# Optimization experiments

Measured on AMD Instinct MI355X. Metric: run time of the kernel, lower is better.

## Reference

```python
import jax, jax.numpy as jnp
import numpy as np

N_HEADS = 12
ROPE_THETA = 10000.0


def _rope(x):
    # x: [B, L, N, D]; interleaved (lucidrains rotary_embedding_torch style) rotation over full D
    B, L, N, D = x.shape
    inv_freq = 1.0 / (ROPE_THETA ** (jnp.arange(0, D, 2, dtype=jnp.float32) / D))  # [D/2]
    freqs = jnp.arange(L, dtype=jnp.float32)[:, None] * inv_freq                    # [L, D/2]
    cos = jnp.repeat(jnp.cos(freqs), 2, axis=-1)[None, :, None, :].astype(x.dtype)  # [1,L,1,D]
    sin = jnp.repeat(jnp.sin(freqs), 2, axis=-1)[None, :, None, :].astype(x.dtype)
    x1 = x[..., 0::2]
    x2 = x[..., 1::2]
    x_rot = jnp.stack([-x2, x1], axis=-1).reshape(x.shape)  # rotate_half, interleaved pairs
    return x * cos + x_rot * sin


def setup_inputs() -> dict:
    key = jax.random.key(0)
    ks = jax.random.split(key, 7)
    B, L, dm = 8, 1024, 768
    x = jax.random.normal(ks[0], (B, L, dm), jnp.float32)
    mask = jax.random.randint(ks[1], (B, L), 0, 2, jnp.int32)          # 1 = keep, 0 = pad
    pos_bias = jax.random.normal(ks[2], (N_HEADS, L, L), jnp.float32) * 0.1
    qkv_w = jax.random.normal(ks[3], (3 * dm, dm), jnp.float32) * 0.02
    qkv_b = jax.random.normal(ks[4], (3 * dm,), jnp.float32) * 0.02
    out_w = jax.random.normal(ks[5], (dm, dm), jnp.float32) * 0.02
    out_b = jax.random.normal(ks[6], (dm,), jnp.float32) * 0.02
    return {"x": x, "pos_bias": pos_bias, "qkv_w": qkv_w, "qkv_b": qkv_b,
            "out_w": out_w, "out_b": out_b, "mask": mask}


def reference(x, pos_bias, qkv_w, qkv_b, out_w, out_b, mask):
    B, L, dm = x.shape
    N = N_HEADS
    D = dm // N
    # QKV projection (torch Linear: y = x @ W.T + b), chunk(3, -1)
    qkv = x @ qkv_w.T + qkv_b                                   # [B, L, 3*dm]
    q, k, v = [a.reshape(B, L, N, D) for a in jnp.split(qkv, 3, axis=-1)]
    q = _rope(q)
    k = _rope(k)
    # scores [B, N, Lq, Lk]
    scores = jnp.einsum('bqnd,bknd->bnqk', q, k) / jnp.sqrt(jnp.asarray(D, x.dtype))
    # mask_to_bias: (mask - 1) with negatives -> -inf, shape [B, 1, 1, L]
    mask_bias = jnp.where(mask > 0, 0.0, -jnp.inf).astype(x.dtype)[:, None, None, :]
    bias = pos_bias[None].astype(x.dtype) + mask_bias           # [B, N, L, L]
    attn = jax.nn.softmax(scores + bias, axis=-1)               # dropout = 0 (eval)
    o = jnp.einsum('bnqk,bknd->bqnd', attn, v).reshape(B, L, dm)
    return o @ out_w.T + out_b
```

## Files before the change

kernel.cpp:

```cpp
#include <hip/hip_runtime.h>

#define DEVINL __device__ __forceinline__

using bf16x8 = __attribute__((ext_vector_type(8))) short;
using f32x4  = __attribute__((ext_vector_type(4))) float;

constexpr int Bb = 8, Ls = 1024, DM = 768, NH = 12, DH = 64;
constexpr int QKV = 3 * DM;

DEVINL unsigned short f2bf(float f) {
    union { float f; unsigned u; } v; v.f = f;
    unsigned r = v.u + 0x7FFFu + ((v.u >> 16) & 1u);
    return (unsigned short)(r >> 16);
}
DEVINL float bf2f(unsigned short h) {
    union { unsigned u; float f; } v; v.u = ((unsigned)h) << 16; return v.f;
}

DEVINL void gload_lds16(const void* g, void* l) {
    __builtin_amdgcn_global_load_lds((const __attribute__((address_space(1))) void*)g,
                                     (__attribute__((address_space(3))) void*)l, 16, 0, 0);
}

__global__ void prep_kernel(const float* __restrict__ x, const float* __restrict__ wq,
                            const float* __restrict__ wo, const float* __restrict__ pbias,
                            unsigned short* __restrict__ xb, unsigned short* __restrict__ wqb,
                            unsigned short* __restrict__ wob, unsigned short* __restrict__ ebb,
                            float* __restrict__ tab) {
    const int X4 = Bb * Ls * DM / 4, W4 = QKV * DM / 4, O4 = DM * DM / 4;
    const int E4 = NH * Ls * Ls / 4, TB = Ls * DH;
    const int total = X4 + W4 + O4 + E4 + TB;
    for (int idx = blockIdx.x * blockDim.x + threadIdx.x; idx < total;
         idx += gridDim.x * blockDim.x) {
        if (idx < X4 + W4 + O4) {
            const float4* s; unsigned short* d; int i;
            if (idx < X4)            { s = (const float4*)x;  d = xb;  i = idx; }
            else if (idx < X4 + W4)  { s = (const float4*)wq; d = wqb; i = idx - X4; }
            else                     { s = (const float4*)wo; d = wob; i = idx - X4 - W4; }
            float4 v = s[i];
            ushort4 o;
            o.x = f2bf(v.x); o.y = f2bf(v.y); o.z = f2bf(v.z); o.w = f2bf(v.w);
            ((ushort4*)d)[i] = o;
        } else if (idx < X4 + W4 + O4 + E4) {
            int i = idx - (X4 + W4 + O4);
            float4 v = ((const float4*)pbias)[i];
            ushort4 o;
            o.x = f2bf(__expf(v.x)); o.y = f2bf(__expf(v.y));
            o.z = f2bf(__expf(v.z)); o.w = f2bf(__expf(v.w));
            ((ushort4*)ebb)[i] = o;
        } else {
            int r = idx - (X4 + W4 + O4 + E4);
            int l = r >> 6, c = r & 63, i = c & 31;
            float freq = powf(10000.0f, -(float)i / 32.0f);
            float ang = (float)l * freq;
            tab[l * 64 + c] = (c < 32) ? cosf(ang) : sinf(ang);
        }
    }
}

template <int OUT_BF16>
__global__ __launch_bounds__(256) void gemm_nt(const unsigned short* __restrict__ A,
                                               const unsigned short* __restrict__ Bw,
                                               const float* __restrict__ bias,
                                               void* __restrict__ Cout,
                                               int M, int Nn, int K) {
    __shared__ unsigned short As[128 * 32];
    __shared__ unsigned short Bs[128 * 32];
    const int tid = threadIdx.x, lane = tid & 63, w = tid >> 6;
    const int bm = blockIdx.x * 128, bn = blockIdx.y * 128;
    const int wm = w >> 1, wn = w & 1;
    const int col = lane & 15, q4 = lane >> 4;
    f32x4 acc[4][4] = {};
    for (int kb = 0; kb < K; kb += 32) {
#pragma unroll
        for (int i = 0; i < 2; ++i) {
            int c0 = w * 128 + i * 64;
            int p = c0 + lane;
            int row = p >> 2;
            int kc = (p & 3) ^ (row & 3);
            gload_lds16(A + (size_t)(bm + row) * K + kb + kc * 8, &As[c0 * 8]);
            gload_lds16(Bw + (size_t)(bn + row) * K + kb + kc * 8, &Bs[c0 * 8]);
        }
        __syncthreads();
        bf16x8 af[4], bfr[4];
#pragma unroll
        for (int t = 0; t < 4; ++t) {
            int ra = wm * 64 + t * 16 + col;
            int rb = wn * 64 + t * 16 + col;
            af[t]  = *(const bf16x8*)&As[(ra * 32 + q4 * 8) ^ ((ra & 3) << 3)];
            bfr[t] = *(const bf16x8*)&Bs[(rb * 32 + q4 * 8) ^ ((rb & 3) << 3)];
        }
#pragma unroll
        for (int t = 0; t < 4; ++t)
#pragma unroll
            for (int u = 0; u < 4; ++u)
                acc[t][u] = __builtin_amdgcn_mfma_f32_16x16x32_bf16(af[t], bfr[u], acc[t][u], 0, 0, 0);
        __syncthreads();
    }
#pragma unroll
    for (int t = 0; t < 4; ++t) {
        int grow_base = bm + wm * 64 + t * 16 + q4 * 4;
#pragma unroll
        for (int u = 0; u < 4; ++u) {
            int gcol = bn + wn * 64 + u * 16 + col;
            float bv = bias[gcol];
#pragma unroll
            for (int r = 0; r < 4; ++r) {
                float vv = acc[t][u][r] + bv;
                if (OUT_BF16)
                    ((unsigned short*)Cout)[(size_t)(grow_base + r) * Nn + gcol] = f2bf(vv);
                else
                    ((float*)Cout)[(size_t)(grow_base + r) * Nn + gcol] = vv;
            }
        }
    }
}

__global__ void rope_qk(const unsigned short* __restrict__ qkvb, const float* __restrict__ tab,
                        unsigned short* __restrict__ qs, unsigned short* __restrict__ ks) {
    const int b = blockIdx.z, n = blockIdx.y;
    const int idx = blockIdx.x * blockDim.x + threadIdx.x;
    const int l = idx >> 3, d8 = idx & 7;
    const float QSCL = 0.125f * 1.44269504089f;
    const unsigned short* src = qkvb + (size_t)(b * Ls + l) * QKV + n * DH + d8 * 8;
    float4 cs = *(const float4*)&tab[l * 64 + d8 * 4];
    float4 sn = *(const float4*)&tab[l * 64 + 32 + d8 * 4];
    float cv[4] = {cs.x, cs.y, cs.z, cs.w};
    float sv[4] = {sn.x, sn.y, sn.z, sn.w};
    size_t dsto = ((size_t)(b * NH + n) * Ls + l) * DH + d8 * 8;
    {
        bf16x8 qv = *(const bf16x8*)src;
        bf16x8 ov;
#pragma unroll
        for (int j = 0; j < 4; ++j) {
            float x1 = bf2f((unsigned short)qv[2 * j]), x2 = bf2f((unsigned short)qv[2 * j + 1]);
            ov[2 * j]     = (short)f2bf((x1 * cv[j] - x2 * sv[j]) * QSCL);
            ov[2 * j + 1] = (short)f2bf((x2 * cv[j] + x1 * sv[j]) * QSCL);
        }
        *(bf16x8*)(qs + dsto) = ov;
    }
    {
        bf16x8 kv = *(const bf16x8*)(src + DM);
        bf16x8 ov;
#pragma unroll
        for (int j = 0; j < 4; ++j) {
            float x1 = bf2f((unsigned short)kv[2 * j]), x2 = bf2f((unsigned short)kv[2 * j + 1]);
            ov[2 * j]     = (short)f2bf(x1 * cv[j] - x2 * sv[j]);
            ov[2 * j + 1] = (short)f2bf(x2 * cv[j] + x1 * sv[j]);
        }
        *(bf16x8*)(ks + dsto) = ov;
    }
}

__global__ void vtrans(const unsigned short* __restrict__ qkvb, unsigned short* __restrict__ vt) {
    __shared__ unsigned short vsh[64][72];
    const int b = blockIdx.z, n = blockIdx.y, lt = blockIdx.x;
    const int tid = threadIdx.x;
#pragma unroll
    for (int i = 0; i < 2; ++i) {
        int c = tid + i * 256;
        int lrow = c >> 3, d8 = c & 7;
        *(bf16x8*)&vsh[lrow][d8 * 8] =
            *(const bf16x8*)(qkvb + (size_t)(b * Ls + lt * 64 + lrow) * QKV + 2 * DM + n * DH + d8 * 8);
    }
    __syncthreads();
#pragma unroll
    for (int i = 0; i < 2; ++i) {
        int c = tid + i * 256;
        int d = c >> 3, l8 = c & 7;
        bf16x8 v;
#pragma unroll
        for (int j = 0; j < 8; ++j) v[j] = (short)vsh[l8 * 8 + j][d];
        *(bf16x8*)(vt + ((size_t)(b * NH + n) * DH + d) * Ls + lt * 64 + l8 * 8) = v;
    }
}

__global__ __launch_bounds__(256) void attn_kernel(const unsigned short* __restrict__ qs,
                                                   const unsigned short* __restrict__ ks,
                                                   const unsigned short* __restrict__ vt,
                                                   const unsigned short* __restrict__ ebb,
                                                   const int* __restrict__ mask,
                                                   unsigned short* __restrict__ ob) {
    __shared__ unsigned short Ksh[64 * 64];
    __shared__ unsigned short Vsh[64 * 64];
    __shared__ unsigned short EBsh[64 * 64];
    __shared__ unsigned short Psh[4][16 * 64];
    __shared__ float maskb[Ls];
    const int b = blockIdx.x, n = blockIdx.y, qt = blockIdx.z;
    const int tid = threadIdx.x, lane = tid & 63, w = tid >> 6;
    const int col = lane & 15, q4 = lane >> 4;
    for (int i = tid; i < Ls; i += 256)
        maskb[i] = (mask[b * Ls + i] > 0) ? 0.0f : -1e30f;
    const unsigned short* qbn = qs + (size_t)(b * NH + n) * Ls * DH;
    const unsigned short* kbn = ks + (size_t)(b * NH + n) * Ls * DH;
    const unsigned short* vbn = vt + (size_t)(b * NH + n) * DH * Ls;
    const unsigned short* ebn = ebb + (size_t)n * Ls * Ls;
    bf16x8 qf[2];
#pragma unroll
    for (int j = 0; j < 2; ++j)
        qf[j] = *(const bf16x8*)(qbn + (size_t)(qt * 64 + w * 16 + col) * DH + q4 * 8 + j * 32);
    const int qrow_c = w * 16 + q4 * 4;
    float psum[4] = {0.f, 0.f, 0.f, 0.f};
    f32x4 oacc[4];
#pragma unroll
    for (int t = 0; t < 4; ++t) oacc[t] = f32x4{0.f, 0.f, 0.f, 0.f};

    for (int kt = 0; kt < Ls / 64; ++kt) {
#pragma unroll
        for (int i = 0; i < 2; ++i) {
            int c0 = w * 128 + i * 64;
            int p = c0 + lane;
            int row = p >> 3, cin = (p & 7) ^ (row & 7);
            gload_lds16(kbn + (size_t)(kt * 64 + row) * DH + cin * 8, &Ksh[c0 * 8]);
            gload_lds16(vbn + (size_t)row * Ls + kt * 64 + cin * 8, &Vsh[c0 * 8]);
            gload_lds16(ebn + (size_t)(qt * 64 + row) * Ls + kt * 64 + cin * 8, &EBsh[c0 * 8]);
        }
        __syncthreads();
        f32x4 s[4];
#pragma unroll
        for (int t = 0; t < 4; ++t) {
            s[t] = f32x4{0.f, 0.f, 0.f, 0.f};
            int krow = t * 16 + col;
#pragma unroll
            for (int j = 0; j < 2; ++j) {
                bf16x8 kf = *(const bf16x8*)&Ksh[(krow * 64 + q4 * 8 + j * 32) ^ ((krow & 7) << 3)];
                s[t] = __builtin_amdgcn_mfma_f32_16x16x32_bf16(qf[j], kf, s[t], 0, 0, 0);
            }
        }
        float p[4][4];
#pragma unroll
        for (int t = 0; t < 4; ++t) {
            int kg = kt * 64 + t * 16 + col;
            float ma = maskb[kg];
            int chunk = t * 2 + (col >> 3);
#pragma unroll
            for (int r = 0; r < 4; ++r) {
                int rowl = qrow_c + r;
                int bo = rowl * 128 + (((chunk ^ (rowl & 7)) << 4)) + ((col & 7) << 1);
                float ebf = bf2f(*(const unsigned short*)((const char*)EBsh + bo));
                float pv = exp2f(s[t][r] + ma) * ebf;
                p[t][r] = pv;
                psum[r] += pv;
            }
        }
        unsigned short* pw = Psh[w];
#pragma unroll
        for (int t = 0; t < 4; ++t)
#pragma unroll
            for (int r = 0; r < 4; ++r) {
                int row = q4 * 4 + r;
                pw[(row * 64 + t * 16 + col) ^ ((row & 7) << 3)] = f2bf(p[t][r]);
            }
#pragma unroll
        for (int ot = 0; ot < 4; ++ot) {
            int vrow = ot * 16 + col;
#pragma unroll
            for (int j = 0; j < 2; ++j) {
                bf16x8 pa = *(const bf16x8*)&pw[(col * 64 + q4 * 8 + j * 32) ^ ((col & 7) << 3)];
                bf16x8 vb = *(const bf16x8*)&Vsh[(vrow * 64 + q4 * 8 + j * 32) ^ ((vrow & 7) << 3)];
                oacc[ot] = __builtin_amdgcn_mfma_f32_16x16x32_bf16(pa, vb, oacc[ot], 0, 0, 0);
            }
        }
        __syncthreads();
    }
#pragma unroll
    for (int r = 0; r < 4; ++r)
#pragma unroll
        for (int msk = 1; msk < 16; msk <<= 1)
            psum[r] += __shfl_xor(psum[r], msk);
#pragma unroll
    for (int r = 0; r < 4; ++r) {
        int lg = qt * 64 + qrow_c + r;
        float inv = 1.0f / psum[r];
#pragma unroll
        for (int ot = 0; ot < 4; ++ot)
            ob[(size_t)(b * Ls + lg) * DM + n * DH + ot * 16 + col] = f2bf(oacc[ot][r] * inv);
    }
}

extern "C" void kernel_launch(void* const* d_in, const int* in_sizes, int n_in,
                              void* d_out, int out_size, void* d_ws, size_t ws_size,
                              hipStream_t stream) {
    const float* x     = (const float*)d_in[0];
    const float* posb  = (const float*)d_in[1];
    const float* qkv_w = (const float*)d_in[2];
    const float* qkv_b = (const float*)d_in[3];
    const float* out_w = (const float*)d_in[4];
    const float* out_b = (const float*)d_in[5];
    const int*   mask  = (const int*)d_in[6];
    float* out = (float*)d_out;

    char* wp = (char*)d_ws;
    auto alloc = [&](size_t bytes) {
        char* p = wp;
        wp += (bytes + 255) & ~(size_t)255;
        return p;
    };
    unsigned short* xb   = (unsigned short*)alloc((size_t)Bb * Ls * DM * 2);
    unsigned short* wqb  = (unsigned short*)alloc((size_t)QKV * DM * 2);
    unsigned short* wob  = (unsigned short*)alloc((size_t)DM * DM * 2);
    unsigned short* ebb  = (unsigned short*)alloc((size_t)NH * Ls * Ls * 2);
    float*          tab  = (float*)alloc((size_t)Ls * DH * 4);
    unsigned short* qkvb = (unsigned short*)alloc((size_t)Bb * Ls * QKV * 2);
    unsigned short* qsb  = (unsigned short*)alloc((size_t)Bb * NH * Ls * DH * 2);
    unsigned short* ksb  = (unsigned short*)alloc((size_t)Bb * NH * Ls * DH * 2);
    unsigned short* vtb  = (unsigned short*)alloc((size_t)Bb * NH * DH * Ls * 2);
    unsigned short* obb  = (unsigned short*)alloc((size_t)Bb * Ls * DM * 2);

    prep_kernel<<<dim3(2048), dim3(256), 0, stream>>>(x, qkv_w, out_w, posb, xb, wqb, wob, ebb, tab);
    gemm_nt<1><<<dim3(64, 18), dim3(256), 0, stream>>>(xb, wqb, qkv_b, (void*)qkvb, Bb * Ls, QKV, DM);
    rope_qk<<<dim3(32, NH, Bb), dim3(256), 0, stream>>>(qkvb, tab, qsb, ksb);
    vtrans<<<dim3(16, NH, Bb), dim3(256), 0, stream>>>(qkvb, vtb);
    attn_kernel<<<dim3(Bb, NH, 16), dim3(256), 0, stream>>>(qsb, ksb, vtb, ebb, mask, obb);
    gemm_nt<0><<<dim3(64, 6), dim3(256), 0, stream>>>(obb, wob, out_b, (void*)out, Bb * Ls, DM, DM);
}
```

Baseline: 294.2 us.

## Double-buffer LDS tiles in GEMM and attention with manual vmcnt waits

Both the projection GEMM and the attention kernel now keep two LDS buffers and prefetch the next K-tile (and next K/V tile) while MFMAs run on the current one, using explicit s_waitcnt vmcnt counts and raw s_barriers instead of __syncthreads. In attention, the bias tile stays single-buffered: its next load is issued once the current tile has been read into registers, which is safe because each wave only loads and reads its own rows. The aim is to hide global-to-LDS latency behind compute. In exchange, LDS use per block goes up, which may cut occupancy, and the hand-counted waitcnts are brittle.

```diff
diff --git a/kernel.cpp b/kernel.cpp
--- a/kernel.cpp
+++ b/kernel.cpp
@@ -64,39 +64,56 @@
                                                const float* __restrict__ bias,
                                                void* __restrict__ Cout,
                                                int M, int Nn, int K) {
-    __shared__ unsigned short As[128 * 32];
-    __shared__ unsigned short Bs[128 * 32];
+    __shared__ unsigned short As[2][128 * 32];
+    __shared__ unsigned short Bs[2][128 * 32];
     const int tid = threadIdx.x, lane = tid & 63, w = tid >> 6;
     const int bm = blockIdx.x * 128, bn = blockIdx.y * 128;
     const int wm = w >> 1, wn = w & 1;
     const int col = lane & 15, q4 = lane >> 4;
     f32x4 acc[4][4] = {};
-    for (int kb = 0; kb < K; kb += 32) {
-#pragma unroll
-        for (int i = 0; i < 2; ++i) {
-            int c0 = w * 128 + i * 64;
-            int p = c0 + lane;
-            int row = p >> 2;
-            int kc = (p & 3) ^ (row & 3);
-            gload_lds16(A + (size_t)(bm + row) * K + kb + kc * 8, &As[c0 * 8]);
-            gload_lds16(Bw + (size_t)(bn + row) * K + kb + kc * 8, &Bs[c0 * 8]);
-        }
-        __syncthreads();
+
+#define GSTAGE(bi, kt_)                                                              \
+    {                                                                                \
+        _Pragma("unroll") for (int i = 0; i < 2; ++i) {                              \
+            int c0 = w * 128 + i * 64;                                               \
+            int p = c0 + lane;                                                       \
+            int row = p >> 2;                                                        \
+            int kc = (p & 3) ^ (row & 3);                                            \
+            gload_lds16(A + (size_t)(bm + row) * K + (kt_)*32 + kc * 8, &As[bi][c0 * 8]); \
+            gload_lds16(Bw + (size_t)(bn + row) * K + (kt_)*32 + kc * 8, &Bs[bi][c0 * 8]); \
+        }                                                                            \
+    }
+
+    const int NT = K / 32;
+    GSTAGE(0, 0);
+    for (int t = 0; t < NT; ++t) {
+        const int cur = t & 1;
+        if (t + 1 < NT) {
+            GSTAGE(cur ^ 1, t + 1);
+            asm volatile("s_waitcnt vmcnt(4)" ::: "memory");
+        } else {
+            asm volatile("s_waitcnt vmcnt(0)" ::: "memory");
+        }
+        __builtin_amdgcn_s_barrier();
+        asm volatile("" ::: "memory");
         bf16x8 af[4], bfr[4];
 #pragma unroll
-        for (int t = 0; t < 4; ++t) {
-            int ra = wm * 64 + t * 16 + col;
-            int rb = wn * 64 + t * 16 + col;
-            af[t]  = *(const bf16x8*)&As[(ra * 32 + q4 * 8) ^ ((ra & 3) << 3)];
-            bfr[t] = *(const bf16x8*)&Bs[(rb * 32 + q4 * 8) ^ ((rb & 3) << 3)];
-        }
-#pragma unroll
-        for (int t = 0; t < 4; ++t)
+        for (int tt = 0; tt < 4; ++tt) {
+            int ra = wm * 64 + tt * 16 + col;
+            int rb = wn * 64 + tt * 16 + col;
+            af[tt]  = *(const bf16x8*)&As[cur][(ra * 32 + q4 * 8) ^ ((ra & 3) << 3)];
+            bfr[tt] = *(const bf16x8*)&Bs[cur][(rb * 32 + q4 * 8) ^ ((rb & 3) << 3)];
+        }
+#pragma unroll
+        for (int tt = 0; tt < 4; ++tt)
 #pragma unroll
             for (int u = 0; u < 4; ++u)
-                acc[t][u] = __builtin_amdgcn_mfma_f32_16x16x32_bf16(af[t], bfr[u], acc[t][u], 0, 0, 0);
-        __syncthreads();
-    }
+                acc[tt][u] = __builtin_amdgcn_mfma_f32_16x16x32_bf16(af[tt], bfr[u], acc[tt][u], 0, 0, 0);
+        __builtin_amdgcn_sched_barrier(0);
+        asm volatile("" ::: "memory");
+        __builtin_amdgcn_s_barrier();
+    }
+#undef GSTAGE
 #pragma unroll
     for (int t = 0; t < 4; ++t) {
         int grow_base = bm + wm * 64 + t * 16 + q4 * 4;
@@ -181,8 +198,8 @@
                                                    const unsigned short* __restrict__ ebb,
                                                    const int* __restrict__ mask,
                                                    unsigned short* __restrict__ ob) {
-    __shared__ unsigned short Ksh[64 * 64];
-    __shared__ unsigned short Vsh[64 * 64];
+    __shared__ unsigned short Ksh[2][64 * 64];
+    __shared__ unsigned short Vsh[2][64 * 64];
     __shared__ unsigned short EBsh[64 * 64];
     __shared__ unsigned short Psh[4][16 * 64];
     __shared__ float maskb[Ls];
@@ -204,18 +221,41 @@
     f32x4 oacc[4];
 #pragma unroll
     for (int t = 0; t < 4; ++t) oacc[t] = f32x4{0.f, 0.f, 0.f, 0.f};
-
-    for (int kt = 0; kt < Ls / 64; ++kt) {
-#pragma unroll
-        for (int i = 0; i < 2; ++i) {
-            int c0 = w * 128 + i * 64;
-            int p = c0 + lane;
-            int row = p >> 3, cin = (p & 7) ^ (row & 7);
-            gload_lds16(kbn + (size_t)(kt * 64 + row) * DH + cin * 8, &Ksh[c0 * 8]);
-            gload_lds16(vbn + (size_t)row * Ls + kt * 64 + cin * 8, &Vsh[c0 * 8]);
-            gload_lds16(ebn + (size_t)(qt * 64 + row) * Ls + kt * 64 + cin * 8, &EBsh[c0 * 8]);
-        }
-        __syncthreads();
+    __syncthreads();
+
+#define STAGE_KV(bi, kt_)                                                                  \
+    {                                                                                      \
+        _Pragma("unroll") for (int i = 0; i < 2; ++i) {                                    \
+            int c0 = w * 128 + i * 64;                                                     \
+            int p = c0 + lane;                                                             \
+            int row = p >> 3, cin = (p & 7) ^ (row & 7);                                   \
+            gload_lds16(kbn + (size_t)((kt_)*64 + row) * DH + cin * 8, &Ksh[bi][c0 * 8]);  \
+            gload_lds16(vbn + (size_t)row * Ls + (kt_)*64 + cin * 8, &Vsh[bi][c0 * 8]);    \
+        }                                                                                  \
+    }
+#define STAGE_EB(kt_)                                                                      \
+    {                                                                                      \
+        _Pragma("unroll") for (int i = 0; i < 2; ++i) {                                    \
+            int c0 = w * 128 + i * 64;                                                     \
+            int p = c0 + lane;                                                             \
+            int row = p >> 3, cin = (p & 7) ^ (row & 7);                                   \
+            gload_lds16(ebn + (size_t)(qt * 64 + row) * Ls + (kt_)*64 + cin * 8, &EBsh[c0 * 8]); \
+        }                                                                                  \
+    }
+
+    const int NT = Ls / 64;
+    STAGE_KV(0, 0);
+    STAGE_EB(0);
+    for (int kt = 0; kt < NT; ++kt) {
+        const int cur = kt & 1;
+        if (kt + 1 < NT) {
+            STAGE_KV(cur ^ 1, kt + 1);
+            asm volatile("s_waitcnt vmcnt(4)" ::: "memory");
+        } else {
+            asm volatile("s_waitcnt vmcnt(0)" ::: "memory");
+        }
+        __builtin_amdgcn_s_barrier();
+        asm volatile("" ::: "memory");
         f32x4 s[4];
 #pragma unroll
         for (int t = 0; t < 4; ++t) {
@@ -223,7 +263,7 @@
             int krow = t * 16 + col;
 #pragma unroll
             for (int j = 0; j < 2; ++j) {
-                bf16x8 kf = *(const bf16x8*)&Ksh[(krow * 64 + q4 * 8 + j * 32) ^ ((krow & 7) << 3)];
+                bf16x8 kf = *(const bf16x8*)&Ksh[cur][(krow * 64 + q4 * 8 + j * 32) ^ ((krow & 7) << 3)];
                 s[t] = __builtin_amdgcn_mfma_f32_16x16x32_bf16(qf[j], kf, s[t], 0, 0, 0);
             }
         }
@@ -243,6 +283,9 @@
                 psum[r] += pv;
             }
         }
+        asm volatile("s_waitcnt lgkmcnt(0)" ::: "memory");
+        __builtin_amdgcn_sched_barrier(0);
+        if (kt + 1 < NT) STAGE_EB(kt + 1);
         unsigned short* pw = Psh[w];
 #pragma unroll
         for (int t = 0; t < 4; ++t)
@@ -257,12 +300,16 @@
 #pragma unroll
             for (int j = 0; j < 2; ++j) {
                 bf16x8 pa = *(const bf16x8*)&pw[(col * 64 + q4 * 8 + j * 32) ^ ((col & 7) << 3)];
-                bf16x8 vb = *(const bf16x8*)&Vsh[(vrow * 64 + q4 * 8 + j * 32) ^ ((vrow & 7) << 3)];
+                bf16x8 vb = *(const bf16x8*)&Vsh[cur][(vrow * 64 + q4 * 8 + j * 32) ^ ((vrow & 7) << 3)];
                 oacc[ot] = __builtin_amdgcn_mfma_f32_16x16x32_bf16(pa, vb, oacc[ot], 0, 0, 0);
             }
         }
-        __syncthreads();
-    }
+        __builtin_amdgcn_sched_barrier(0);
+        asm volatile("" ::: "memory");
+        __builtin_amdgcn_s_barrier();
+    }
+#undef STAGE_KV
+#undef STAGE_EB
 #pragma unroll
     for (int r = 0; r < 4; ++r)
 #pragma unroll
```

Result: faster. 285.5 us (-2.9%).
